# Performance work log

Measured on AMD Instinct MI355X. Metric: run time of the kernel, lower is better.

## Reference

```python
import jax, jax.numpy as jnp
import numpy as np
from jax import lax

STRIDE = 1
PAD = 1


def _unfold(x, k, stride, padding):
    # torch.nn.functional.unfold: patches ordered (c, kh, kw), channel slowest
    N, C, H, W = x.shape
    xp = jnp.pad(x, ((0, 0), (0, 0), (padding, padding), (padding, padding)))
    Ho = (H - k + 2 * padding) // stride + 1
    Wo = (W - k + 2 * padding) // stride + 1
    cols = [xp[:, :, i:i + stride * Ho:stride, j:j + stride * Wo:stride]
            for i in range(k) for j in range(k)]  # k*k slices of (N,C,Ho,Wo)
    p = jnp.stack(cols, axis=2)  # (N, C, k*k, Ho, Wo) -> (c, kh, kw) ordering
    return p.reshape(N, C * k * k, Ho * Wo), Ho, Wo


def setup_inputs() -> dict:
    key = jax.random.key(0)
    k1, k2 = jax.random.split(key)
    x = jax.random.normal(k1, (16, 128, 28, 28), dtype=jnp.float32)
    W = jax.random.normal(k2, (256, 128, 3, 3), dtype=jnp.float32)
    return {"x": x, "W": W}


def reference(x, W):
    O, C, k, _ = W.shape
    N = x.shape[0]
    Xc, Ho, Wo = _unfold(x, k, STRIDE, PAD)          # (N, d, L)
    d = C * k * k
    Xp = Xc.transpose(0, 2, 1).reshape(N * Ho * Wo, d)  # (P, d), P = N*Ho*Wo
    Wf = W.reshape(O, d)                               # (O, d)
    # out[f, p] = -sum_d |W[f,d] - X[p,d]|  (AdderNet: -cdist(W, X, p=1))
    # Stream over filters to avoid the O*P*d pairwise buffer.
    out = -lax.map(lambda w: jnp.sum(jnp.abs(w[None, :] - Xp), axis=-1), Wf)  # (O, P)
    return out.reshape(O, N, Ho, Wo).transpose(1, 0, 2, 3)  # (N, O, Ho, Wo)
```

## Files before the change

### kernel.cpp

```cpp
#include <hip/hip_runtime.h>


typedef unsigned int u32;

#define WD 28
#define HW 784
#define CIN 128
#define OUT_F 256
#define TN 8
#define NW 8
#define C4PW 4
#define WL_N (32 * 9 * TN)
#define SSTR 31
#define SLAB_N (16 * SSTR)

#define QSCALE 23.0f
#define QBIAS  127.0f
#define PADB   0x7F7F7F7Fu

static __device__ __forceinline__ u32 quant4(float a, float b, float c, float d) {
#if __has_builtin(__builtin_amdgcn_cvt_pk_u8_f32)
    u32 p = 0;
    p = __builtin_amdgcn_cvt_pk_u8_f32(fmaf(a, QSCALE, QBIAS), 0, p);
    p = __builtin_amdgcn_cvt_pk_u8_f32(fmaf(b, QSCALE, QBIAS), 1, p);
    p = __builtin_amdgcn_cvt_pk_u8_f32(fmaf(c, QSCALE, QBIAS), 2, p);
    p = __builtin_amdgcn_cvt_pk_u8_f32(fmaf(d, QSCALE, QBIAS), 3, p);
    return p;
#else
    auto q1 = [](float v) -> u32 {
        float t = fmaf(v, QSCALE, QBIAS);
        t = fminf(fmaxf(t, 0.f), 255.f);
        return (u32)(t + 0.5f);
    };
    return q1(a) | (q1(b) << 8) | (q1(c) << 16) | (q1(d) << 24);
#endif
}

static __device__ __forceinline__ u32 sad4(u32 a, u32 b, u32 acc) {
#if __has_builtin(__builtin_amdgcn_sad_u8)
    return __builtin_amdgcn_sad_u8(a, b, acc);
#else
    #pragma unroll
    for (int i = 0; i < 4; ++i) {
        const int av = (a >> (8 * i)) & 0xFF;
        const int bv = (b >> (8 * i)) & 0xFF;
        acc += (u32)((av > bv) ? (av - bv) : (bv - av));
    }
    return acc;
#endif
}

__global__ __launch_bounds__(512, 2) void adder2d_kernel(
    const float* __restrict__ x,
    const float* __restrict__ Wf,
    float* __restrict__ out)
{
    __shared__ u32 Wl[WL_N];
    __shared__ __align__(16) u32 Xs[NW][SLAB_N];

    const int tid  = threadIdx.x;
    const int bx   = blockIdx.x;
    const int n    = bx >> 1;
    const int hb   = bx & 1;
    const int h0   = hb * 14;
    const int f0   = blockIdx.y * TN;
    const int wid  = tid >> 6;
    const int lane = tid & 63;
    const int kb   = wid * C4PW;

    #pragma unroll
    for (int k = 0; k < 5; ++k) {
        const int m = tid + k * 512;
        if (m < WL_N) {
            const int ff = m & 7;
            const int q  = m >> 3;
            const int s  = q % 9;
            const int c4 = q / 9;
            const float* b = Wf + ((size_t)(f0 + ff) * CIN + 4 * c4) * 9 + s;
            Wl[m] = quant4(b[0], b[9], b[18], b[27]);
        }
    }
    if (lane < 32) {
        const int r = lane >> 1, sd = lane & 1;
        Xs[wid][r * SSTR + (sd ? 29 : 0)] = PADB;
    }

    const float* xn = x + (size_t)n * CIN * HW;
    float lv[4][4];

    #define STAGE(c4g)                                                        \
        {                                                                     \
            const float* xc = xn + (size_t)(4 * (c4g)) * HW;                  \
            _Pragma("unroll")                                                 \
            for (int k = 0; k < 4; ++k) {                                     \
                const int slot = lane + k * 64;                               \
                const int r = slot / 28, w = slot - r * 28;                   \
                const int h = h0 - 1 + r;                                     \
                if (h >= 0 && h < WD) {                                       \
                    const float* p = xc + h * WD + w;                         \
                    lv[k][0] = p[0];      lv[k][1] = p[HW];                   \
                    lv[k][2] = p[2 * HW]; lv[k][3] = p[3 * HW];               \
                }                                                             \
            }                                                                 \
            _Pragma("unroll")                                                 \
            for (int k = 0; k < 4; ++k) {                                     \
                const int slot = lane + k * 64;                               \
                const int r = slot / 28, w = slot - r * 28;                   \
                const int h = h0 - 1 + r;                                     \
                u32 qv = PADB;                                                \
                if (h >= 0 && h < WD)                                         \
                    qv = quant4(lv[k][0], lv[k][1], lv[k][2], lv[k][3]);      \
                Xs[wid][r * SSTR + w + 1] = qv;                               \
            }                                                                 \
            _Pragma("unroll")                                                 \
            for (int k = 4; k < 7; ++k) {                                     \
                const int slot = lane + k * 64;                               \
                const int r = slot / 28, w = slot - r * 28;                   \
                const int h = h0 - 1 + r;                                     \
                if (h >= 0 && h < WD) {                                       \
                    const float* p = xc + h * WD + w;                         \
                    lv[k - 4][0] = p[0];      lv[k - 4][1] = p[HW];           \
                    lv[k - 4][2] = p[2 * HW]; lv[k - 4][3] = p[3 * HW];       \
                }                                                             \
            }                                                                 \
            _Pragma("unroll")                                                 \
            for (int k = 4; k < 7; ++k) {                                     \
                const int slot = lane + k * 64;                               \
                const int r = slot / 28, w = slot - r * 28;                   \
                const int h = h0 - 1 + r;                                     \
                u32 qv = PADB;                                                \
                if (h >= 0 && h < WD)                                         \
                    qv = quant4(lv[k - 4][0], lv[k - 4][1],                   \
                                lv[k - 4][2], lv[k - 4][3]);                  \
                Xs[wid][r * SSTR + w + 1] = qv;                               \
            }                                                                 \
        }

    STAGE(kb);
    __syncthreads();

    const bool active = lane < 56;
    const int row = lane >> 2;
    const int cs  = (lane & 3) * 7;

    u32 acc[7][TN] = {};

    #pragma unroll 1
    for (int l = 0; l < C4PW; ++l) {
        if (active) {
            const u32* sb = &Xs[wid][row * SSTR + cs];
            u32 xv[3][9];
            #pragma unroll
            for (int i = 0; i < 3; ++i)
                #pragma unroll
                for (int j = 0; j < 9; ++j)
                    xv[i][j] = sb[i * SSTR + j];
            const uint4* wq = reinterpret_cast<const uint4*>(&Wl[(kb + l) * 72]);
            #pragma unroll
            for (int kh = 0; kh < 3; ++kh) {
                #pragma unroll
                for (int kw = 0; kw < 3; ++kw) {
                    const int s = kh * 3 + kw;
                    const uint4 wa = wq[2 * s];
                    const uint4 wb = wq[2 * s + 1];
                    #pragma unroll
                    for (int pc = 0; pc < 7; ++pc) {
                        const u32 xs = xv[kh][kw + pc];
                        acc[pc][0] = sad4(wa.x, xs, acc[pc][0]);
                        acc[pc][1] = sad4(wa.y, xs, acc[pc][1]);
                        acc[pc][2] = sad4(wa.z, xs, acc[pc][2]);
                        acc[pc][3] = sad4(wa.w, xs, acc[pc][3]);
                        acc[pc][4] = sad4(wb.x, xs, acc[pc][4]);
                        acc[pc][5] = sad4(wb.y, xs, acc[pc][5]);
                        acc[pc][6] = sad4(wb.z, xs, acc[pc][6]);
                        acc[pc][7] = sad4(wb.w, xs, acc[pc][7]);
                    }
                }
            }
        }
        if (l + 1 < C4PW) STAGE(kb + l + 1);
    }
    __syncthreads();

    u32* scr = &Xs[0][0];
    #pragma unroll
    for (int c = 0; c < 4; ++c) {
        const int fb = 2 * c;
        if ((wid & 1) && active) {
            #pragma unroll
            for (int g = 0; g < 2; ++g)
                #pragma unroll
                for (int pc = 0; pc < 7; ++pc)
                    scr[(wid >> 1) * 960 + lane * 15 + g * 7 + pc] = acc[pc][fb + g];
        }
        __syncthreads();
        if (!(wid & 1) && active) {
            #pragma unroll
            for (int g = 0; g < 2; ++g)
                #pragma unroll
                for (int pc = 0; pc < 7; ++pc)
                    acc[pc][fb + g] += scr[(wid >> 1) * 960 + lane * 15 + g * 7 + pc];
        }
        __syncthreads();
        if ((wid == 2 || wid == 6) && active) {
            #pragma unroll
            for (int g = 0; g < 2; ++g)
                #pragma unroll
                for (int pc = 0; pc < 7; ++pc)
                    scr[(wid >> 2) * 960 + lane * 15 + g * 7 + pc] = acc[pc][fb + g];
        }
        __syncthreads();
        if ((wid == 0 || wid == 4) && active) {
            #pragma unroll
            for (int g = 0; g < 2; ++g)
                #pragma unroll
                for (int pc = 0; pc < 7; ++pc)
                    acc[pc][fb + g] += scr[(wid >> 2) * 960 + lane * 15 + g * 7 + pc];
        }
        __syncthreads();
        if (wid == 4 && active) {
            #pragma unroll
            for (int g = 0; g < 2; ++g)
                #pragma unroll
                for (int pc = 0; pc < 7; ++pc)
                    scr[lane * 15 + g * 7 + pc] = acc[pc][fb + g];
        }
        __syncthreads();
        if (wid == 0 && active) {
            #pragma unroll
            for (int g = 0; g < 2; ++g)
                #pragma unroll
                for (int pc = 0; pc < 7; ++pc)
                    acc[pc][fb + g] += scr[lane * 15 + g * 7 + pc];
        }
        __syncthreads();
    }

    if (wid == 0 && active) {
        const float sc = -(1.0f / QSCALE);
        const int ho = h0 + row;
        float* ob = out + (size_t)n * OUT_F * HW + ho * WD + cs;
        #pragma unroll
        for (int ff = 0; ff < TN; ++ff) {
            float* o = ob + (size_t)(f0 + ff) * HW;
            #pragma unroll
            for (int pc = 0; pc < 7; ++pc)
                o[pc] = (float)acc[pc][ff] * sc;
        }
    }
}

extern "C" void kernel_launch(void* const* d_in, const int* in_sizes, int n_in,
                              void* d_out, int out_size, void* d_ws, size_t ws_size,
                              hipStream_t stream) {
    const float* x  = (const float*)d_in[0];
    const float* Wf = (const float*)d_in[1];
    float* out = (float*)d_out;

    dim3 grid(32, OUT_F / TN);
    adder2d_kernel<<<grid, dim3(512), 0, stream>>>(x, Wf, out);
}
```

Measured before the change: 55.21 us.

## Halve block to 4 waves with 8 channel groups each and shorter reduction

Each block now runs 4 wavefronts instead of 8, and each wave processes 8 channel-quad groups instead of 4. The cross-wave reduction drops from three levels to two and runs in 3 filter chunks with a new scratch stride. Weights and slabs now share one shared-memory array, which the reduction reuses as scratch. The aim is fewer barriers and less reduction traffic per block, and possibly more resident blocks per CU, at the cost of a longer serial inner loop per wave and less latency hiding within a block.

Result: no change. 54.68 us (median of 2 runs) (-1.0%).

```diff
diff --git a/kernel.cpp b/kernel.cpp
--- a/kernel.cpp
+++ b/kernel.cpp
@@ -8,11 +8,12 @@
 #define CIN 128
 #define OUT_F 256
 #define TN 8
-#define NW 8
-#define C4PW 4
+#define NW 4
+#define C4PW 8
 #define WL_N (32 * 9 * TN)
 #define SSTR 31
 #define SLAB_N (16 * SSTR)
+#define S_TOT (WL_N + NW * SLAB_N)
 
 #define QSCALE 23.0f
 #define QBIAS  127.0f
@@ -50,13 +51,14 @@
 #endif
 }
 
-__global__ __launch_bounds__(512, 2) void adder2d_kernel(
+__global__ __launch_bounds__(256, 2) void adder2d_kernel(
     const float* __restrict__ x,
     const float* __restrict__ Wf,
     float* __restrict__ out)
 {
-    __shared__ u32 Wl[WL_N];
-    __shared__ __align__(16) u32 Xs[NW][SLAB_N];
+    __shared__ __align__(16) u32 S[S_TOT];
+
+    u32* const Wl = S;
 
     const int tid  = threadIdx.x;
     const int bx   = blockIdx.x;
@@ -68,21 +70,21 @@
     const int lane = tid & 63;
     const int kb   = wid * C4PW;
 
+    u32* const slab = S + WL_N + wid * SLAB_N;
+
     #pragma unroll
-    for (int k = 0; k < 5; ++k) {
-        const int m = tid + k * 512;
-        if (m < WL_N) {
-            const int ff = m & 7;
-            const int q  = m >> 3;
-            const int s  = q % 9;
-            const int c4 = q / 9;
-            const float* b = Wf + ((size_t)(f0 + ff) * CIN + 4 * c4) * 9 + s;
-            Wl[m] = quant4(b[0], b[9], b[18], b[27]);
-        }
+    for (int k = 0; k < 9; ++k) {
+        const int m  = tid + k * 256;
+        const int ff = m & 7;
+        const int q  = m >> 3;
+        const int s  = q % 9;
+        const int c4 = q / 9;
+        const float* b = Wf + ((size_t)(f0 + ff) * CIN + 4 * c4) * 9 + s;
+        Wl[m] = quant4(b[0], b[9], b[18], b[27]);
     }
     if (lane < 32) {
         const int r = lane >> 1, sd = lane & 1;
-        Xs[wid][r * SSTR + (sd ? 29 : 0)] = PADB;
+        slab[r * SSTR + (sd ? 29 : 0)] = PADB;
     }
 
     const float* xn = x + (size_t)n * CIN * HW;
@@ -110,7 +112,7 @@
                 u32 qv = PADB;                                                \
                 if (h >= 0 && h < WD)                                         \
                     qv = quant4(lv[k][0], lv[k][1], lv[k][2], lv[k][3]);      \
-                Xs[wid][r * SSTR + w + 1] = qv;                               \
+                slab[r * SSTR + w + 1] = qv;                                  \
             }                                                                 \
             _Pragma("unroll")                                                 \
             for (int k = 4; k < 7; ++k) {                                     \
@@ -132,7 +134,7 @@
                 if (h >= 0 && h < WD)                                         \
                     qv = quant4(lv[k - 4][0], lv[k - 4][1],                   \
                                 lv[k - 4][2], lv[k - 4][3]);                  \
-                Xs[wid][r * SSTR + w + 1] = qv;                               \
+                slab[r * SSTR + w + 1] = qv;                                  \
             }                                                                 \
         }
 
@@ -148,7 +150,7 @@
     #pragma unroll 1
     for (int l = 0; l < C4PW; ++l) {
         if (active) {
-            const u32* sb = &Xs[wid][row * SSTR + cs];
+            const u32* sb = &slab[row * SSTR + cs];
             u32 xv[3][9];
             #pragma unroll
             for (int i = 0; i < 3; ++i)
@@ -182,56 +184,44 @@
     }
     __syncthreads();
 
-    u32* scr = &Xs[0][0];
+    #define MSTR 23
+    u32* scr = S;
     #pragma unroll
-    for (int c = 0; c < 4; ++c) {
-        const int fb = 2 * c;
+    for (int c = 0; c < 3; ++c) {
+        const int fb = c * 3;
+        const int nf = (c == 2) ? 2 : 3;
         if ((wid & 1) && active) {
             #pragma unroll
-            for (int g = 0; g < 2; ++g)
-                #pragma unroll
-                for (int pc = 0; pc < 7; ++pc)
-                    scr[(wid >> 1) * 960 + lane * 15 + g * 7 + pc] = acc[pc][fb + g];
+            for (int g = 0; g < 3; ++g) if (g < nf)
+                #pragma unroll
+                for (int pc = 0; pc < 7; ++pc)
+                    scr[(wid >> 1) * (64 * MSTR) + lane * MSTR + g * 7 + pc]
+                        = acc[pc][fb + g];
         }
         __syncthreads();
         if (!(wid & 1) && active) {
             #pragma unroll
-            for (int g = 0; g < 2; ++g)
-                #pragma unroll
-                for (int pc = 0; pc < 7; ++pc)
-                    acc[pc][fb + g] += scr[(wid >> 1) * 960 + lane * 15 + g * 7 + pc];
-        }
-        __syncthreads();
-        if ((wid == 2 || wid == 6) && active) {
-            #pragma unroll
-            for (int g = 0; g < 2; ++g)
-                #pragma unroll
-                for (int pc = 0; pc < 7; ++pc)
-                    scr[(wid >> 2) * 960 + lane * 15 + g * 7 + pc] = acc[pc][fb + g];
-        }
-        __syncthreads();
-        if ((wid == 0 || wid == 4) && active) {
-            #pragma unroll
-            for (int g = 0; g < 2; ++g)
-                #pragma unroll
-                for (int pc = 0; pc < 7; ++pc)
-                    acc[pc][fb + g] += scr[(wid >> 2) * 960 + lane * 15 + g * 7 + pc];
-        }
-        __syncthreads();
-        if (wid == 4 && active) {
-            #pragma unroll
-            for (int g = 0; g < 2; ++g)
-                #pragma unroll
-                for (int pc = 0; pc < 7; ++pc)
-                    scr[lane * 15 + g * 7 + pc] = acc[pc][fb + g];
+            for (int g = 0; g < 3; ++g) if (g < nf)
+                #pragma unroll
+                for (int pc = 0; pc < 7; ++pc)
+                    acc[pc][fb + g] +=
+                        scr[(wid >> 1) * (64 * MSTR) + lane * MSTR + g * 7 + pc];
+        }
+        __syncthreads();
+        if (wid == 2 && active) {
+            #pragma unroll
+            for (int g = 0; g < 3; ++g) if (g < nf)
+                #pragma unroll
+                for (int pc = 0; pc < 7; ++pc)
+                    scr[lane * MSTR + g * 7 + pc] = acc[pc][fb + g];
         }
         __syncthreads();
         if (wid == 0 && active) {
             #pragma unroll
-            for (int g = 0; g < 2; ++g)
-                #pragma unroll
-                for (int pc = 0; pc < 7; ++pc)
-                    acc[pc][fb + g] += scr[lane * 15 + g * 7 + pc];
+            for (int g = 0; g < 3; ++g) if (g < nf)
+                #pragma unroll
+                for (int pc = 0; pc < 7; ++pc)
+                    acc[pc][fb + g] += scr[lane * MSTR + g * 7 + pc];
         }
         __syncthreads();
     }
@@ -258,5 +248,5 @@
     float* out = (float*)d_out;
 
     dim3 grid(32, OUT_F / TN);
-    adder2d_kernel<<<grid, dim3(512), 0, stream>>>(x, Wf, out);
-}
+    adder2d_kernel<<<grid, dim3(256), 0, stream>>>(x, Wf, out);
+}
```
